# Kernel optimization log

Hardware: AMD Instinct MI355X
Metric: run time of the kernel (lower is better)

The kernel has to match this reference:

```python
import jax, jax.numpy as jnp
import numpy as np

EMBED_DIM = 1024
NUM_HEADS = 16
HEAD_DIM = EMBED_DIM // NUM_HEADS
LN_EPS = 1e-5


def setup_inputs() -> dict:
    key = jax.random.key(0)
    ks = jax.random.split(key, 13)
    b, n_q, k_len, E = 4, 2048, 2048, EMBED_DIM
    s = 1.0 / np.sqrt(E)
    inp = {
        "Q_input": jax.random.normal(ks[0], (b, n_q, E), jnp.float32),
        "K_input": jax.random.normal(ks[1], (b, k_len, E), jnp.float32),
        "V_input": jax.random.normal(ks[2], (b, k_len, E), jnp.float32),
        "Wq": jax.random.normal(ks[3], (E, E), jnp.float32) * s,
        "bq": jnp.zeros((E,), jnp.float32),
        "Wk": jax.random.normal(ks[4], (E, E), jnp.float32) * s,
        "bk": jnp.zeros((E,), jnp.float32),
        "Wv": jax.random.normal(ks[5], (E, E), jnp.float32) * s,
        "bv": jnp.zeros((E,), jnp.float32),
        "Wo": jax.random.normal(ks[6], (E, E), jnp.float32) * s,
        "bo": jnp.zeros((E,), jnp.float32),
        "gamma": jnp.ones((E,), jnp.float32),
        "beta": jnp.zeros((E,), jnp.float32),
    }
    return inp


def _layer_norm(x, gamma, beta):
    mu = jnp.mean(x, axis=-1, keepdims=True)
    var = jnp.mean(jnp.square(x - mu), axis=-1, keepdims=True)
    return (x - mu) * jax.lax.rsqrt(var + LN_EPS) * gamma + beta


def reference(Q_input, K_input, V_input, Wq, bq, Wk, bk, Wv, bv, Wo, bo, gamma, beta):
    b, n_q, E = Q_input.shape
    k_len = K_input.shape[1]
    H, D = NUM_HEADS, HEAD_DIM
    # projections (Linear: x @ W^T + b; here W stored as [E_in, E_out])
    Q = (Q_input @ Wq + bq).reshape(b, n_q, H, D).transpose(0, 2, 1, 3)   # [b,H,n_q,D]
    K = (K_input @ Wk + bk).reshape(b, k_len, H, D).transpose(0, 2, 1, 3)  # [b,H,k,D]
    V = (V_input @ Wv + bv).reshape(b, k_len, H, D).transpose(0, 2, 1, 3)
    scores = jnp.einsum('bhqd,bhkd->bhqk', Q, K) / jnp.sqrt(jnp.float32(D))
    attn = jax.nn.softmax(scores, axis=-1)
    ctx = jnp.einsum('bhqk,bhkd->bhqd', attn, V)           # [b,H,n_q,D]
    ctx = ctx.transpose(0, 2, 1, 3).reshape(b, n_q, E)
    out = ctx @ Wo + bo                                    # dropout = identity (eval)
    return _layer_norm(Q_input + out, gamma, beta)
```

## Files before the change

kernel.cpp:

```cpp
#include <hip/hip_runtime.h>

typedef __attribute__((ext_vector_type(8))) short s8v;
typedef __attribute__((ext_vector_type(4))) short s4v;
typedef __attribute__((ext_vector_type(4))) float f4v;

#define MFMA16(a, b, c) __builtin_amdgcn_mfma_f32_16x16x32_bf16((a), (b), (c), 0, 0, 0)
#define AS1 __attribute__((address_space(1)))
#define AS3 __attribute__((address_space(3)))

__device__ __forceinline__ short f2bf(float f) {
  union { float f; unsigned u; } v; v.f = f;
  unsigned r = v.u + 0x7FFFu + ((v.u >> 16) & 1u);
  return (short)(r >> 16);
}
__device__ __forceinline__ float bf2f(short s) {
  union { unsigned u; float f; } v; v.u = ((unsigned)(unsigned short)s) << 16;
  return v.f;
}
__device__ __forceinline__ unsigned fbits(float f) {
  union { float f; unsigned u; } v; v.f = f; return v.u;
}
__device__ __forceinline__ unsigned pack2(float hi, float lo) {
  return __builtin_amdgcn_perm(fbits(hi), fbits(lo), 0x07060302u);
}
__device__ __forceinline__ unsigned pack2rn(float hi, float lo) {
  return __builtin_amdgcn_perm(fbits(hi) + 0x8000u, fbits(lo) + 0x8000u, 0x07060302u);
}
__device__ __forceinline__ void gld16(const void* g, void* l) {
  __builtin_amdgcn_global_load_lds((const AS1 unsigned*)g, (AS3 unsigned*)l, 16, 0, 0);
}

__global__ __launch_bounds__(256) void wtrans4(const float* __restrict__ W0,
                                               const float* __restrict__ W1,
                                               const float* __restrict__ W2,
                                               const float* __restrict__ W3,
                                               short* __restrict__ Wt) {
  const float* W = blockIdx.z == 0 ? W0 : blockIdx.z == 1 ? W1 : blockIdx.z == 2 ? W2 : W3;
  Wt += (size_t)blockIdx.z * 1048576;
  __shared__ float tile[64][65];
  const int r0 = blockIdx.y * 64, c0 = blockIdx.x * 64;
  const int t = threadIdx.x;
  for (int i = 0; i < 4; ++i) {
    int lin = t + i * 256;
    int row = lin >> 4, c4 = (lin & 15) << 2;
    float4 v = *(const float4*)(W + (size_t)(r0 + row) * 1024 + c0 + c4);
    tile[row][c4 + 0] = v.x; tile[row][c4 + 1] = v.y;
    tile[row][c4 + 2] = v.z; tile[row][c4 + 3] = v.w;
  }
  __syncthreads();
  for (int i = 0; i < 4; ++i) {
    int lin = t + i * 256;
    int nl = lin >> 4, k4 = (lin & 15) << 2;
    s4v sv = { f2bf(tile[k4 + 0][nl]), f2bf(tile[k4 + 1][nl]),
               f2bf(tile[k4 + 2][nl]), f2bf(tile[k4 + 3][nl]) };
    *(s4v*)&Wt[(size_t)(c0 + nl) * 1024 + r0 + k4] = sv;
  }
}

__global__ __launch_bounds__(256) void cast_a(const float* __restrict__ A0,
                                              const float* __restrict__ A1,
                                              const float* __restrict__ A2,
                                              short* __restrict__ outb) {
  const float* A = blockIdx.y == 0 ? A0 : blockIdx.y == 1 ? A1 : A2;
  short* o = outb + (size_t)blockIdx.y * 8388608;
  const size_t base = ((size_t)blockIdx.x * 256 + threadIdx.x) * 16;
  const float4 v0 = *(const float4*)(A + base);
  const float4 v1 = *(const float4*)(A + base + 4);
  const float4 v2 = *(const float4*)(A + base + 8);
  const float4 v3 = *(const float4*)(A + base + 12);
  union { s8v v; unsigned u[4]; } p0, p1;
  p0.u[0] = pack2rn(v0.y, v0.x); p0.u[1] = pack2rn(v0.w, v0.z);
  p0.u[2] = pack2rn(v1.y, v1.x); p0.u[3] = pack2rn(v1.w, v1.z);
  p1.u[0] = pack2rn(v2.y, v2.x); p1.u[1] = pack2rn(v2.w, v2.z);
  p1.u[2] = pack2rn(v3.y, v3.x); p1.u[3] = pack2rn(v3.w, v3.z);
  *(s8v*)(o + base) = p0.v;
  *(s8v*)(o + base + 8) = p1.v;
}

template <int EPI>
__global__ __launch_bounds__(256) void gemm_bt(
    const short* __restrict__ Ab, const short* __restrict__ Bt,
    const float* __restrict__ b0, const float* __restrict__ b1,
    const float* __restrict__ b2, float s0,
    short* __restrict__ outb) {
  __shared__ __align__(16) short smem[17408];

  const int z = blockIdx.z;
  Ab += (size_t)z * 8388608;
  Bt += (size_t)z * 1048576;
  outb += (size_t)z * 8388608;
  const float* bias = z == 0 ? b0 : z == 1 ? b1 : b2;
  const float scale = z == 0 ? s0 : 1.f;

  const int tid = threadIdx.x;
  const int lane = tid & 63, w = tid >> 6;
  const int quad = lane >> 4, l16 = lane & 15;
  const int wm = (w >> 1) * 64, wn = (w & 1) * 64;
  const int mBase = blockIdx.x * 128, nBase = blockIdx.y * 128;
  f4v acc[4][4] = {};

  const int id0 = tid, id1 = tid + 256;
  const short* Bg0 = Bt + (size_t)((id0 >> 2) + nBase) * 1024 + ((id0 & 3) << 3);
  const short* Bg1 = Bt + (size_t)((id1 >> 2) + nBase) * 1024 + ((id1 & 3) << 3);
  const short* Ag0 = Ab + (size_t)((id0 >> 2) + mBase) * 1024 + ((id0 & 3) << 3);
  const short* Ag1 = Ab + (size_t)((id1 >> 2) + mBase) * 1024 + ((id1 & 3) << 3);

  gld16(Ag0, &smem[id0 * 8]);
  gld16(Ag1, &smem[id1 * 8]);
  gld16(Bg0, &smem[4096 + id0 * 8]);
  gld16(Bg1, &smem[4096 + id1 * 8]);

  for (int kt = 0; kt < 32; ++kt) {
    const int bo_ = (kt & 1) * 8192, nbo = bo_ ^ 8192;
    __syncthreads();
    if (kt < 31) {
      gld16(Bg0 + (kt + 1) * 32, &smem[nbo + 4096 + id0 * 8]);
      gld16(Bg1 + (kt + 1) * 32, &smem[nbo + 4096 + id1 * 8]);
      gld16(Ag0 + (kt + 1) * 32, &smem[nbo + id0 * 8]);
      gld16(Ag1 + (kt + 1) * 32, &smem[nbo + id1 * 8]);
    }
    s8v a[4], b[4];
#pragma unroll
    for (int mt = 0; mt < 4; ++mt) a[mt] = *(const s8v*)&smem[bo_ + (wm + mt * 16 + l16) * 32 + quad * 8];
#pragma unroll
    for (int nt = 0; nt < 4; ++nt) b[nt] = *(const s8v*)&smem[bo_ + 4096 + (wn + nt * 16 + l16) * 32 + quad * 8];
#pragma unroll
    for (int mt = 0; mt < 4; ++mt)
#pragma unroll
      for (int nt = 0; nt < 4; ++nt)
        acc[mt][nt] = MFMA16(a[mt], b[nt], acc[mt][nt]);
  }

  __syncthreads();
  const int bI = mBase >> 11, tok0 = mBase & 2047;
  const bool vpath = (EPI == 0) && (z == 2);
  short (*Ta)[136] = (short(*)[136])smem;
  short (*Tv)[136] = (short(*)[136])smem;
  if (vpath) {
#pragma unroll
    for (int nt = 0; nt < 4; ++nt) {
      int featl = wn + nt * 16 + l16;
      float bs = bias[nBase + featl];
#pragma unroll
      for (int mt = 0; mt < 4; ++mt) {
        union { s4v v; unsigned u[2]; } pk;
        pk.u[0] = pack2(acc[mt][nt][1] + bs, acc[mt][nt][0] + bs);
        pk.u[1] = pack2(acc[mt][nt][3] + bs, acc[mt][nt][2] + bs);
        *(s4v*)&Tv[featl][wm + mt * 16 + quad * 4] = pk.v;
      }
    }
  } else {
#pragma unroll
    for (int nt = 0; nt < 4; ++nt) {
      int featl = wn + nt * 16 + l16;
      float bs = bias[nBase + featl];
#pragma unroll
      for (int mt = 0; mt < 4; ++mt)
#pragma unroll
        for (int r = 0; r < 4; ++r)
          Ta[wm + mt * 16 + quad * 4 + r][featl] = f2bf((acc[mt][nt][r] + bs) * scale);
    }
  }
  __syncthreads();
  if (vpath) {
#pragma unroll
    for (int it = 0; it < 8; ++it) {
      int id = tid + it * 256;
      int f = id >> 4, t8 = (id & 15) << 3;
      s8v v = *(const s8v*)&Tv[f][t8];
      int gf = nBase + f, h = gf >> 6, d = gf & 63;
      *(s8v*)&outb[(((size_t)bI * 16 + h) * 64 + d) * 2048 + tok0 + t8] = v;
    }
  } else {
#pragma unroll
    for (int it = 0; it < 8; ++it) {
      int id = tid + it * 256;
      int tok = id >> 4, f8 = (id & 15) << 3;
      s8v v = *(const s8v*)&Ta[tok][f8];
      if constexpr (EPI == 1) {
        *(s8v*)&outb[(size_t)(mBase + tok) * 1024 + nBase + f8] = v;
      } else {
        int gf = nBase + f8, h = gf >> 6, d = gf & 63;
        *(s8v*)&outb[(((size_t)bI * 16 + h) * 2048 + tok0 + tok) * 64 + d] = v;
      }
    }
  }
}

__global__ __launch_bounds__(256, 2) void attn_kernel(
    const short* __restrict__ Qp, const short* __restrict__ Kp,
    const short* __restrict__ Vpt, short* __restrict__ Ctx) {
  __shared__ __align__(16) short Ks[2][64][72];
  __shared__ __align__(16) short Vt[2][64][72];

  const int tid = threadIdx.x, w = tid >> 6, lane = tid & 63;
  const int quad = lane >> 4, l16 = lane & 15;
  const int qt = blockIdx.x, bh = blockIdx.y;
  const short* Qb = Qp + (size_t)bh * 2048 * 64;
  const short* Kb = Kp + (size_t)bh * 2048 * 64;
  const short* Vb = Vpt + (size_t)bh * 64 * 2048;
  const int qbase = qt * 256 + w * 64;

  int sg[2], sc8[2], sp[2];
  const short* Ksrc[2];
  const short* Vsrc[2];
#pragma unroll
  for (int i = 0; i < 2; ++i) {
    int id = tid + i * 256;
    int g = id >> 3, c8 = (id & 7) << 3;
    int p = (g & 32) | (((g >> 2) & 1) << 4) | (((g >> 3) & 3) << 2) | (g & 3);
    sg[i] = g; sc8[i] = c8; sp[i] = p;
    Ksrc[i] = Kb + (size_t)g * 64 + c8;
    Vsrc[i] = Vb + (size_t)g * 2048 + c8;
  }

  s8v qf[4][2];
#pragma unroll
  for (int mt = 0; mt < 4; ++mt)
#pragma unroll
    for (int h = 0; h < 2; ++h)
      qf[mt][h] = *(const s8v*)(Qb + (size_t)(qbase + mt * 16 + l16) * 64 + h * 32 + quad * 8);

  {
    s8v kr[2], vr[2];
#pragma unroll
    for (int i = 0; i < 2; ++i) { kr[i] = *(const s8v*)Ksrc[i]; vr[i] = *(const s8v*)Vsrc[i]; }
#pragma unroll
    for (int i = 0; i < 2; ++i) {
      *(s8v*)&Ks[0][sp[i]][sc8[i]] = kr[i];
      *(s8v*)&Vt[0][sg[i]][sc8[i]] = vr[i];
    }
  }

  const s8v vone = {16256, 16256, 16256, 16256, 16256, 16256, 16256, 16256};
  f4v Oa[4][4] = {};
  f4v La[4] = {};

  for (int kv = 0; kv < 32; ++kv) {
    const int buf = kv & 1;
    s8v kn[2], vn[2];
    if (kv < 31) {
#pragma unroll
      for (int i = 0; i < 2; ++i) {
        kn[i] = *(const s8v*)(Ksrc[i] + (size_t)(kv + 1) * 4096);
        vn[i] = *(const s8v*)(Vsrc[i] + (size_t)(kv + 1) * 64);
      }
    }
    __syncthreads();

    s8v kf[4][2], vf[4][2];
#pragma unroll
    for (int T = 0; T < 4; ++T) {
      kf[T][0] = *(const s8v*)&Ks[buf][T * 16 + l16][quad * 8];
      kf[T][1] = *(const s8v*)&Ks[buf][T * 16 + l16][32 + quad * 8];
      vf[T][0] = *(const s8v*)&Vt[buf][T * 16 + l16][quad * 8];
      vf[T][1] = *(const s8v*)&Vt[buf][T * 16 + l16][32 + quad * 8];
    }

#pragma unroll
    for (int mt = 0; mt < 4; ++mt) {
      f4v s[4] = {};
#pragma unroll
      for (int T = 0; T < 4; ++T) {
        s[T] = MFMA16(kf[T][0], qf[mt][0], s[T]);
        s[T] = MFMA16(kf[T][1], qf[mt][1], s[T]);
      }
#pragma unroll
      for (int T = 0; T < 4; ++T)
#pragma unroll
        for (int r = 0; r < 4; ++r)
          s[T][r] = __builtin_amdgcn_exp2f(s[T][r]);
      s8v pf[2];
#pragma unroll
      for (int cp = 0; cp < 2; ++cp) {
        union { s8v v; unsigned u[4]; } pk;
        pk.u[0] = pack2(s[2 * cp][1], s[2 * cp][0]);
        pk.u[1] = pack2(s[2 * cp][3], s[2 * cp][2]);
        pk.u[2] = pack2(s[2 * cp + 1][1], s[2 * cp + 1][0]);
        pk.u[3] = pack2(s[2 * cp + 1][3], s[2 * cp + 1][2]);
        pf[cp] = pk.v;
      }
      La[mt] = MFMA16(pf[0], vone, La[mt]);
      La[mt] = MFMA16(pf[1], vone, La[mt]);
#pragma unroll
      for (int nt = 0; nt < 4; ++nt) {
        Oa[mt][nt] = MFMA16(pf[0], vf[nt][0], Oa[mt][nt]);
        Oa[mt][nt] = MFMA16(pf[1], vf[nt][1], Oa[mt][nt]);
      }
    }

    if (kv < 31) {
#pragma unroll
      for (int i = 0; i < 2; ++i) {
        *(s8v*)&Ks[buf ^ 1][sp[i]][sc8[i]] = kn[i];
        *(s8v*)&Vt[buf ^ 1][sg[i]][sc8[i]] = vn[i];
      }
    }
  }

  const int b = bh >> 4, h = bh & 15;
#pragma unroll
  for (int mt = 0; mt < 4; ++mt)
#pragma unroll
    for (int r = 0; r < 4; ++r) {
      float inv = 1.f / La[mt][r];
      int q = qbase + mt * 16 + quad * 4 + r;
#pragma unroll
      for (int nt = 0; nt < 4; ++nt) {
        int d = nt * 16 + l16;
        Ctx[((size_t)b * 2048 + q) * 1024 + h * 64 + d] = f2bf(Oa[mt][nt][r] * inv);
      }
    }
}

__global__ __launch_bounds__(256) void ln_kernel(
    const float* __restrict__ resid, const short* __restrict__ attnb,
    const float* __restrict__ gamma, const float* __restrict__ beta,
    float* __restrict__ out) {
  const int row = blockIdx.x, t = threadIdx.x;
  const float4 rv = *(const float4*)(resid + (size_t)row * 1024 + t * 4);
  const s4v av = *(const s4v*)(attnb + (size_t)row * 1024 + t * 4);
  float x0 = rv.x + bf2f(av[0]), x1 = rv.y + bf2f(av[1]);
  float x2 = rv.z + bf2f(av[2]), x3 = rv.w + bf2f(av[3]);
  float s = x0 + x1 + x2 + x3;
  float ss = x0 * x0 + x1 * x1 + x2 * x2 + x3 * x3;
  for (int off = 32; off > 0; off >>= 1) {
    s += __shfl_down(s, off, 64);
    ss += __shfl_down(ss, off, 64);
  }
  __shared__ float red[8];
  const int wid = t >> 6, lane = t & 63;
  if (lane == 0) { red[wid] = s; red[4 + wid] = ss; }
  __syncthreads();
  float S = red[0] + red[1] + red[2] + red[3];
  float SS = red[4] + red[5] + red[6] + red[7];
  float mu = S * (1.f / 1024.f);
  float var = SS * (1.f / 1024.f) - mu * mu;
  float rstd = rsqrtf(var + 1e-5f);
  const float4 g = *(const float4*)(gamma + t * 4);
  const float4 bb = *(const float4*)(beta + t * 4);
  float4 o;
  o.x = (x0 - mu) * rstd * g.x + bb.x;
  o.y = (x1 - mu) * rstd * g.y + bb.y;
  o.z = (x2 - mu) * rstd * g.z + bb.z;
  o.w = (x3 - mu) * rstd * g.w + bb.w;
  *(float4*)(out + (size_t)row * 1024 + t * 4) = o;
}

extern "C" void kernel_launch(void* const* d_in, const int* in_sizes, int n_in,
                              void* d_out, int out_size, void* d_ws, size_t ws_size,
                              hipStream_t stream) {
  const float* Qin = (const float*)d_in[0];
  const float* Kin = (const float*)d_in[1];
  const float* Vin = (const float*)d_in[2];
  const float* Wq = (const float*)d_in[3];
  const float* bq = (const float*)d_in[4];
  const float* Wk = (const float*)d_in[5];
  const float* bk = (const float*)d_in[6];
  const float* Wv = (const float*)d_in[7];
  const float* bv = (const float*)d_in[8];
  const float* Wo = (const float*)d_in[9];
  const float* bo = (const float*)d_in[10];
  const float* gamma = (const float*)d_in[11];
  const float* beta = (const float*)d_in[12];
  float* out = (float*)d_out;

  char* ws = (char*)d_ws;
  const size_t MB = 1024 * 1024;
  short* Qp    = (short*)(ws);
  short* Acast = (short*)(ws + 48 * MB);
  short* Ctx   = (short*)(ws + 48 * MB);
  short* AOutB = (short*)(ws + 64 * MB);
  short* Wt    = (short*)(ws + 96 * MB);

  wtrans4<<<dim3(16, 16, 4), 256, 0, stream>>>(Wq, Wk, Wv, Wo, Wt);
  cast_a<<<dim3(2048, 3), 256, 0, stream>>>(Qin, Kin, Vin, Acast);

  const float qscale = 0.125f * 1.44269504f;

  gemm_bt<0><<<dim3(64, 8, 3), 256, 0, stream>>>(
      Acast, Wt, bq, bk, bv, qscale, Qp);

  attn_kernel<<<dim3(8, 64), 256, 0, stream>>>(Qp, Qp + 8388608, Qp + 16777216, Ctx);

  gemm_bt<1><<<dim3(64, 8, 1), 256, 0, stream>>>(
      Ctx, Wt + 3 * 1048576, bo, bo, bo, 1.f, AOutB);

  ln_kernel<<<8192, 256, 0, stream>>>(Qin, AOutB, gamma, beta, out);
}
```

Before: 348.2 us.

## Rewrite projection GEMM as 8-wave 128x256 tile with triple-buffered pipelined loads

```diff
diff --git a/kernel.cpp b/kernel.cpp
--- a/kernel.cpp
+++ b/kernel.cpp
@@ -77,13 +77,16 @@
   *(s8v*)(o + base + 8) = p1.v;
 }
 
+#define GLDA(j, bb, kt) gld16(Asrc[j] + (size_t)(kt) * 64, &smem[(bb) + ldsA + (j) * 4096])
+#define GLDB(j, bb, kt) gld16(Bsrc[j] + (size_t)(kt) * 64, &smem[(bb) + 8192 + ldsA + (j) * 4096])
+
 template <int EPI>
-__global__ __launch_bounds__(256) void gemm_bt(
+__global__ __launch_bounds__(512, 2) void gemm8p(
     const short* __restrict__ Ab, const short* __restrict__ Bt,
     const float* __restrict__ b0, const float* __restrict__ b1,
     const float* __restrict__ b2, float s0,
     short* __restrict__ outb) {
-  __shared__ __align__(16) short smem[17408];
+  __shared__ __align__(16) short smem[73728];
 
   const int z = blockIdx.z;
   Ab += (size_t)z * 8388608;
@@ -95,87 +98,164 @@
   const int tid = threadIdx.x;
   const int lane = tid & 63, w = tid >> 6;
   const int quad = lane >> 4, l16 = lane & 15;
-  const int wm = (w >> 1) * 64, wn = (w & 1) * 64;
-  const int mBase = blockIdx.x * 128, nBase = blockIdx.y * 128;
+  const int wm = (w >> 2) * 64, wn = (w & 3) * 64;
+  const int mBase = blockIdx.x * 128, nBase = blockIdx.y * 256;
+
   f4v acc[4][4] = {};
 
-  const int id0 = tid, id1 = tid + 256;
-  const short* Bg0 = Bt + (size_t)((id0 >> 2) + nBase) * 1024 + ((id0 & 3) << 3);
-  const short* Bg1 = Bt + (size_t)((id1 >> 2) + nBase) * 1024 + ((id1 & 3) << 3);
-  const short* Ag0 = Ab + (size_t)((id0 >> 2) + mBase) * 1024 + ((id0 & 3) << 3);
-  const short* Ag1 = Ab + (size_t)((id1 >> 2) + mBase) * 1024 + ((id1 & 3) << 3);
-
-  gld16(Ag0, &smem[id0 * 8]);
-  gld16(Ag1, &smem[id1 * 8]);
-  gld16(Bg0, &smem[4096 + id0 * 8]);
-  gld16(Bg1, &smem[4096 + id1 * 8]);
-
-  for (int kt = 0; kt < 32; ++kt) {
-    const int bo_ = (kt & 1) * 8192, nbo = bo_ ^ 8192;
-    __syncthreads();
-    if (kt < 31) {
-      gld16(Bg0 + (kt + 1) * 32, &smem[nbo + 4096 + id0 * 8]);
-      gld16(Bg1 + (kt + 1) * 32, &smem[nbo + 4096 + id1 * 8]);
-      gld16(Ag0 + (kt + 1) * 32, &smem[nbo + id0 * 8]);
-      gld16(Ag1 + (kt + 1) * 32, &smem[nbo + id1 * 8]);
-    }
-    s8v a[4], b[4];
-#pragma unroll
-    for (int mt = 0; mt < 4; ++mt) a[mt] = *(const s8v*)&smem[bo_ + (wm + mt * 16 + l16) * 32 + quad * 8];
-#pragma unroll
-    for (int nt = 0; nt < 4; ++nt) b[nt] = *(const s8v*)&smem[bo_ + 4096 + (wn + nt * 16 + l16) * 32 + quad * 8];
-#pragma unroll
-    for (int mt = 0; mt < 4; ++mt)
-#pragma unroll
-      for (int nt = 0; nt < 4; ++nt)
-        acc[mt][nt] = MFMA16(a[mt], b[nt], acc[mt][nt]);
-  }
-
-  __syncthreads();
+  const short* Asrc[2];
+  const short* Bsrc[4];
+#pragma unroll
+  for (int j = 0; j < 2; ++j) {
+    int s = tid + j * 512;
+    Asrc[j] = Ab + (size_t)(mBase + (s >> 3)) * 1024 + (((s & 7) ^ ((s >> 3) & 7)) << 3);
+  }
+#pragma unroll
+  for (int j = 0; j < 4; ++j) {
+    int s = tid + j * 512;
+    Bsrc[j] = Bt + (size_t)(nBase + (s >> 3)) * 1024 + (((s & 7) ^ ((s >> 3) & 7)) << 3);
+  }
+  const int ldsA = tid * 8;
+
+  int axk[2];
+#pragma unroll
+  for (int kh = 0; kh < 2; ++kh) axk[kh] = (((kh * 4 + quad) ^ (l16 & 7)) << 3);
+  const int arow = (wm + l16) * 64;
+  const int brow = 8192 + (wn + l16) * 64;
+
+#pragma unroll
+  for (int t = 0; t < 3; ++t) {
+    const int bb = t * 24576;
+    GLDB(0, bb, t); GLDB(1, bb, t); GLDB(2, bb, t); GLDB(3, bb, t);
+    GLDA(0, bb, t); GLDA(1, bb, t);
+  }
+  asm volatile("s_waitcnt vmcnt(12)" ::: "memory");
+  __builtin_amdgcn_s_barrier();
+
+  int cb = 0, sb = 49152;
+#pragma unroll 1
+  for (int kt = 0; kt < 16; ++kt) {
+    const bool st = (kt + 2) < 16;
+    s8v a[4][2], b[4][2];
+#pragma unroll
+    for (int kh = 0; kh < 2; ++kh) {
+      b[0][kh] = *(const s8v*)&smem[cb + brow + 0 * 1024 + axk[kh]];
+      b[1][kh] = *(const s8v*)&smem[cb + brow + 1 * 1024 + axk[kh]];
+      a[0][kh] = *(const s8v*)&smem[cb + arow + 0 * 1024 + axk[kh]];
+      a[1][kh] = *(const s8v*)&smem[cb + arow + 1 * 1024 + axk[kh]];
+    }
+    if (st) { GLDB(0, sb, kt + 2); GLDB(1, sb, kt + 2); }
+    __builtin_amdgcn_s_barrier();
+    __builtin_amdgcn_s_setprio(1);
+#pragma unroll
+    for (int nt = 0; nt < 2; ++nt)
+#pragma unroll
+      for (int mt = 0; mt < 2; ++mt)
+#pragma unroll
+        for (int kh = 0; kh < 2; ++kh)
+          acc[nt][mt] = MFMA16(b[nt][kh], a[mt][kh], acc[nt][mt]);
+    __builtin_amdgcn_s_setprio(0);
+    __builtin_amdgcn_s_barrier();
+#pragma unroll
+    for (int kh = 0; kh < 2; ++kh) {
+      b[2][kh] = *(const s8v*)&smem[cb + brow + 2 * 1024 + axk[kh]];
+      b[3][kh] = *(const s8v*)&smem[cb + brow + 3 * 1024 + axk[kh]];
+    }
+    if (st) { GLDB(2, sb, kt + 2); GLDB(3, sb, kt + 2); }
+    __builtin_amdgcn_s_barrier();
+    __builtin_amdgcn_s_setprio(1);
+#pragma unroll
+    for (int nt = 2; nt < 4; ++nt)
+#pragma unroll
+      for (int mt = 0; mt < 2; ++mt)
+#pragma unroll
+        for (int kh = 0; kh < 2; ++kh)
+          acc[nt][mt] = MFMA16(b[nt][kh], a[mt][kh], acc[nt][mt]);
+    __builtin_amdgcn_s_setprio(0);
+    __builtin_amdgcn_s_barrier();
+#pragma unroll
+    for (int kh = 0; kh < 2; ++kh) {
+      a[2][kh] = *(const s8v*)&smem[cb + arow + 2 * 1024 + axk[kh]];
+      a[3][kh] = *(const s8v*)&smem[cb + arow + 3 * 1024 + axk[kh]];
+    }
+    if (st) { GLDA(0, sb, kt + 2); }
+    __builtin_amdgcn_s_barrier();
+    __builtin_amdgcn_s_setprio(1);
+#pragma unroll
+    for (int nt = 2; nt < 4; ++nt)
+#pragma unroll
+      for (int mt = 2; mt < 4; ++mt)
+#pragma unroll
+        for (int kh = 0; kh < 2; ++kh)
+          acc[nt][mt] = MFMA16(b[nt][kh], a[mt][kh], acc[nt][mt]);
+    __builtin_amdgcn_s_setprio(0);
+    __builtin_amdgcn_s_barrier();
+    if (st) { GLDA(1, sb, kt + 2); }
+    __builtin_amdgcn_s_barrier();
+    __builtin_amdgcn_s_setprio(1);
+#pragma unroll
+    for (int nt = 0; nt < 2; ++nt)
+#pragma unroll
+      for (int mt = 2; mt < 4; ++mt)
+#pragma unroll
+        for (int kh = 0; kh < 2; ++kh)
+          acc[nt][mt] = MFMA16(b[nt][kh], a[mt][kh], acc[nt][mt]);
+    __builtin_amdgcn_s_setprio(0);
+    if (kt < 14) {
+      asm volatile("s_waitcnt vmcnt(6)" ::: "memory");
+    } else if (kt == 14) {
+      asm volatile("s_waitcnt vmcnt(0)" ::: "memory");
+    }
+    if (kt < 15) __builtin_amdgcn_s_barrier();
+    cb = (cb == 49152) ? 0 : cb + 24576;
+    sb = (sb == 49152) ? 0 : sb + 24576;
+  }
+
+  f4v bv_[4];
+#pragma unroll
+  for (int nt = 0; nt < 4; ++nt)
+    bv_[nt] = *(const f4v*)&bias[nBase + wn + nt * 16 + quad * 4];
+
   const int bI = mBase >> 11, tok0 = mBase & 2047;
   const bool vpath = (EPI == 0) && (z == 2);
-  short (*Ta)[136] = (short(*)[136])smem;
-  short (*Tv)[136] = (short(*)[136])smem;
   if (vpath) {
-#pragma unroll
-    for (int nt = 0; nt < 4; ++nt) {
-      int featl = wn + nt * 16 + l16;
-      float bs = bias[nBase + featl];
-#pragma unroll
-      for (int mt = 0; mt < 4; ++mt) {
-        union { s4v v; unsigned u[2]; } pk;
-        pk.u[0] = pack2(acc[mt][nt][1] + bs, acc[mt][nt][0] + bs);
-        pk.u[1] = pack2(acc[mt][nt][3] + bs, acc[mt][nt][2] + bs);
-        *(s4v*)&Tv[featl][wm + mt * 16 + quad * 4] = pk.v;
-      }
-    }
-  } else {
-#pragma unroll
-    for (int nt = 0; nt < 4; ++nt) {
-      int featl = wn + nt * 16 + l16;
-      float bs = bias[nBase + featl];
-#pragma unroll
-      for (int mt = 0; mt < 4; ++mt)
-#pragma unroll
-        for (int r = 0; r < 4; ++r)
-          Ta[wm + mt * 16 + quad * 4 + r][featl] = f2bf((acc[mt][nt][r] + bs) * scale);
-    }
-  }
-  __syncthreads();
-  if (vpath) {
+    short (*Tv)[136] = (short(*)[136])smem;
+#pragma unroll
+    for (int nt = 0; nt < 4; ++nt)
+#pragma unroll
+      for (int r = 0; r < 4; ++r) {
+        int feat = wn + nt * 16 + quad * 4 + r;
+#pragma unroll
+        for (int mt = 0; mt < 4; ++mt)
+          Tv[feat][wm + mt * 16 + l16] = f2bf(acc[nt][mt][r] + bv_[nt][r]);
+      }
+    __syncthreads();
 #pragma unroll
     for (int it = 0; it < 8; ++it) {
-      int id = tid + it * 256;
+      int id = tid + it * 512;
       int f = id >> 4, t8 = (id & 15) << 3;
       s8v v = *(const s8v*)&Tv[f][t8];
       int gf = nBase + f, h = gf >> 6, d = gf & 63;
       *(s8v*)&outb[(((size_t)bI * 16 + h) * 64 + d) * 2048 + tok0 + t8] = v;
     }
   } else {
+    short (*Ta)[264] = (short(*)[264])smem;
+#pragma unroll
+    for (int nt = 0; nt < 4; ++nt)
+#pragma unroll
+      for (int mt = 0; mt < 4; ++mt) {
+        union { s4v v; unsigned u[2]; } pk;
+        pk.u[0] = pack2rn((acc[nt][mt][1] + bv_[nt][1]) * scale,
+                          (acc[nt][mt][0] + bv_[nt][0]) * scale);
+        pk.u[1] = pack2rn((acc[nt][mt][3] + bv_[nt][3]) * scale,
+                          (acc[nt][mt][2] + bv_[nt][2]) * scale);
+        *(s4v*)&Ta[wm + mt * 16 + l16][wn + nt * 16 + quad * 4] = pk.v;
+      }
+    __syncthreads();
 #pragma unroll
     for (int it = 0; it < 8; ++it) {
-      int id = tid + it * 256;
-      int tok = id >> 4, f8 = (id & 15) << 3;
+      int id = tid + it * 512;
+      int tok = id >> 5, f8 = (id & 31) << 3;
       s8v v = *(const s8v*)&Ta[tok][f8];
       if constexpr (EPI == 1) {
         *(s8v*)&outb[(size_t)(mBase + tok) * 1024 + nBase + f8] = v;
@@ -378,12 +458,12 @@
 
   const float qscale = 0.125f * 1.44269504f;
 
-  gemm_bt<0><<<dim3(64, 8, 3), 256, 0, stream>>>(
+  gemm8p<0><<<dim3(64, 4, 3), 512, 0, stream>>>(
       Acast, Wt, bq, bk, bv, qscale, Qp);
 
   attn_kernel<<<dim3(8, 64), 256, 0, stream>>>(Qp, Qp + 8388608, Qp + 16777216, Ctx);
 
-  gemm_bt<1><<<dim3(64, 8, 1), 256, 0, stream>>>(
+  gemm8p<1><<<dim3(64, 4, 1), 512, 0, stream>>>(
       Ctx, Wt + 3 * 1048576, bo, bo, bo, 1.f, AOutB);
 
   ln_kernel<<<8192, 256, 0, stream>>>(Qin, AOutB, gamma, beta, out);
```

Measured after the change: 337.3 us. 3.1% less time.
